# Performance work log

Measured on AMD Instinct MI355X. Metric: run time of the kernel, lower is better.

Reference implementation:

```python
import jax, jax.numpy as jnp
import numpy as np

D_MODEL = 1024
NUM_HEADS = 16
HEAD_DIM = D_MODEL // NUM_HEADS


def setup_inputs() -> dict:
    key = jax.random.key(0)
    ks = jax.random.split(key, 5)
    B, S = 4, 2048
    scale = 0.02
    return {
        "x": jax.random.normal(ks[0], (B, S, D_MODEL), dtype=jnp.float32),
        "q_proj_weight": jax.random.normal(ks[1], (D_MODEL, D_MODEL), dtype=jnp.float32) * scale,
        "k_proj_weight": jax.random.normal(ks[2], (D_MODEL, D_MODEL), dtype=jnp.float32) * scale,
        "v_proj_weight": jax.random.normal(ks[3], (D_MODEL, D_MODEL), dtype=jnp.float32) * scale,
        "o_proj_weight": jax.random.normal(ks[4], (D_MODEL, D_MODEL), dtype=jnp.float32) * scale,
    }


def reference(x, q_proj_weight, k_proj_weight, v_proj_weight, o_proj_weight):
    B, S, _ = x.shape
    H, Dh = NUM_HEADS, HEAD_DIM

    def proj(w):  # [B,S,d_model] x [d_k,d_in] -> [B,H,S,Dh]
        p = jnp.einsum('bsd,kd->bsk', x, w)
        return p.reshape(B, S, H, Dh).transpose(0, 2, 1, 3)

    q = proj(q_proj_weight)
    k = proj(k_proj_weight)
    v = proj(v_proj_weight)

    scores = jnp.einsum('bhqd,bhkd->bhqk', q, k) / jnp.sqrt(jnp.asarray(Dh, dtype=x.dtype))
    causal = jnp.tril(jnp.ones((S, S), dtype=bool))  # [S,S]
    scores = jnp.where(causal, scores, -jnp.inf)
    attn = jax.nn.softmax(scores, axis=-1)
    out = jnp.einsum('bhqk,bhkd->bhqd', attn, v)  # [B,H,S,Dh]
    out = out.transpose(0, 2, 1, 3).reshape(B, S, D_MODEL)
    return jnp.einsum('bsv,mv->bsm', out, o_proj_weight)
```

## Files before the change

kernel.cpp:

```cpp
#include <hip/hip_runtime.h>
#include <cstdint>
#include <cstddef>

#define NH 16
#define DH 64
#define SEQ 2048
#define DM 1024

typedef __attribute__((ext_vector_type(8))) short short8;
typedef __attribute__((ext_vector_type(4))) float f32x4;

__device__ __forceinline__ unsigned short f2bf(float f) {
  unsigned u = __builtin_bit_cast(unsigned, f);
  u += 0x7fffu + ((u >> 16) & 1u);
  return (unsigned short)(u >> 16);
}

__device__ __forceinline__ void gld_lds16(const void* g, void* l) {
  __builtin_amdgcn_global_load_lds((const __attribute__((address_space(1))) void*)g,
                                   (__attribute__((address_space(3))) void*)l,
                                   16, 0, 0);
}

__global__ __launch_bounds__(256) void cast_all_kernel(const float* __restrict__ x,
                                                       const float* __restrict__ wq,
                                                       const float* __restrict__ wk,
                                                       const float* __restrict__ wv,
                                                       const float* __restrict__ wo,
                                                       unsigned short* __restrict__ xb,
                                                       unsigned short* __restrict__ wqkvb,
                                                       unsigned short* __restrict__ wob) {
  const int bid = blockIdx.x;
  const float* in;
  unsigned short* out;
  int i;
  if (bid < 8192) {
    in = x; out = xb; i = bid * 256 + threadIdx.x;
  } else {
    const int w = (bid - 8192) >> 10;
    i = ((bid - 8192) & 1023) * 256 + threadIdx.x;
    in = (w == 0) ? wq : (w == 1) ? wk : (w == 2) ? wv : wo;
    out = (w < 3) ? (wqkvb + (size_t)w * 1048576) : wob;
  }
  const float4 v = ((const float4*)in)[i];
  ushort4 o;
  o.x = f2bf(v.x); o.y = f2bf(v.y); o.z = f2bf(v.z); o.w = f2bf(v.w);
  ((ushort4*)out)[i] = o;
}

__global__ __launch_bounds__(512, 2) void gemm_qkv256(const unsigned short* __restrict__ A,
                                                      const unsigned short* __restrict__ W,
                                                      unsigned short* __restrict__ qb,
                                                      unsigned short* __restrict__ kb,
                                                      unsigned short* __restrict__ vtb) {
  extern __shared__ __align__(16) char sm[];

  const int t = threadIdx.x;
  const int lane = t & 63;
  const int wave = t >> 6;
  const int quad = lane >> 4;
  const int l16 = lane & 15;
  const int wr = wave >> 2;
  const int wc = wave & 3;

  const int bid = blockIdx.x;
  const int xcd = bid & 7;
  const int idx = bid >> 3;
  const int bm = (xcd * 4 + idx / 12) * 256;
  const int bn = (idx % 12) * 256;
  const int sel = bn >> 10;
  const int bnl = bn & 1023;

  f32x4 acc[8][4];
#pragma unroll
  for (int i = 0; i < 8; ++i)
#pragma unroll
    for (int j = 0; j < 4; ++j) acc[i][j] = {0.0f, 0.0f, 0.0f, 0.0f};

  const int r0s = t >> 3;
  const int g0 = (((t & 7) ^ (r0s & 7)) * 8);
  const unsigned short* aS0 = A + (size_t)(bm + r0s) * DM + g0;
  const unsigned short* aS1 = A + (size_t)(bm + 64 + r0s) * DM + g0;
  const unsigned short* bS0 = W + (size_t)(bn + r0s) * DM + g0;
  const unsigned short* bS1 = W + (size_t)(bn + 64 + r0s) * DM + g0;
  const int t16 = t * 16;

  const int aswz = (quad ^ (l16 & 7)) * 16;
  const int aRd0 = (wr * 128 + l16) * 128 + aswz;
  const int aRd1 = aRd0 ^ 64;
  const int bRd0 = 65536 + (wc * 64 + l16) * 128 + aswz;
  const int bRd1 = bRd0 ^ 64;

#define ST_A(U, TK, PAR)                                                                   \
  {                                                                                        \
    gld_lds16(aS0 + (size_t)(U) * 131072 + (TK) * 64, sm + (PAR) * 32768 + (U) * 16384 + t16); \
    gld_lds16(aS1 + (size_t)(U) * 131072 + (TK) * 64,                                      \
              sm + (PAR) * 32768 + (U) * 16384 + 8192 + t16);                              \
  }
#define ST_B(U, TK, PAR)                                                                   \
  {                                                                                        \
    gld_lds16(bS0 + (size_t)(U) * 131072 + (TK) * 64,                                      \
              sm + 65536 + (PAR) * 32768 + (U) * 16384 + t16);                             \
    gld_lds16(bS1 + (size_t)(U) * 131072 + (TK) * 64,                                      \
              sm + 65536 + (PAR) * 32768 + (U) * 16384 + 8192 + t16);                      \
  }

#define MM(AF, BF, IB, JB)                                                                 \
  _Pragma("unroll")                                                                        \
  for (int i = 0; i < 4; ++i)                                                              \
    _Pragma("unroll")                                                                      \
    for (int j = 0; j < 2; ++j) {                                                          \
      acc[(IB) + i][(JB) + j] = __builtin_amdgcn_mfma_f32_16x16x32_bf16(                   \
          AF[i][0], BF[j][0], acc[(IB) + i][(JB) + j], 0, 0, 0);                           \
      acc[(IB) + i][(JB) + j] = __builtin_amdgcn_mfma_f32_16x16x32_bf16(                   \
          AF[i][1], BF[j][1], acc[(IB) + i][(JB) + j], 0, 0, 0);                           \
    }

#define TILE(T, PAR, SB, SA, VM)                                                           \
  {                                                                                        \
    short8 af0[4][2], af1[4][2], bf0[2][2], bf1[2][2];                                     \
                                          \
    _Pragma("unroll")                                                                      \
    for (int i = 0; i < 4; ++i) {                                                          \
      af0[i][0] = *(const short8*)(sm + (PAR) * 32768 + i * 2048 + aRd0);                  \
      af0[i][1] = *(const short8*)(sm + (PAR) * 32768 + i * 2048 + aRd1);                  \
    }                                                                                      \
    _Pragma("unroll")                                                                      \
    for (int j = 0; j < 2; ++j) {                                                          \
      bf0[j][0] = *(const short8*)(sm + (PAR) * 32768 + j * 2048 + bRd0);                  \
      bf0[j][1] = *(const short8*)(sm + (PAR) * 32768 + j * 2048 + bRd1);                  \
    }                                                                                      \
    if (SB) ST_B(0, (T) + 1, (PAR) ^ 1);                                                   \
    asm volatile("" ::: "memory");                                                         \
    __builtin_amdgcn_s_barrier();                                                          \
    asm volatile("s_waitcnt lgkmcnt(0)" ::: "memory");                                     \
    __builtin_amdgcn_s_setprio(1);                                                         \
    MM(af0, bf0, 0, 0);                                                                    \
    __builtin_amdgcn_s_setprio(0);                                                         \
    asm volatile("" ::: "memory");                                                         \
    __builtin_amdgcn_s_barrier();                                                          \
                                                     \
    _Pragma("unroll")                                                                      \
    for (int i = 0; i < 4; ++i) {                                                          \
      af1[i][0] = *(const short8*)(sm + (PAR) * 32768 + 8192 + i * 2048 + aRd0);           \
      af1[i][1] = *(const short8*)(sm + (PAR) * 32768 + 8192 + i * 2048 + aRd1);           \
    }                                                                                      \
    if (SB) ST_B(1, (T) + 1, (PAR) ^ 1);                                                   \
    asm volatile("" ::: "memory");                                                         \
    __builtin_amdgcn_s_barrier();                                                          \
    asm volatile("s_waitcnt lgkmcnt(0)" ::: "memory");                                     \
    __builtin_amdgcn_s_setprio(1);                                                         \
    MM(af1, bf0, 4, 0);                                                                    \
    __builtin_amdgcn_s_setprio(0);                                                         \
    asm volatile("" ::: "memory");                                                         \
    __builtin_amdgcn_s_barrier();                                                          \
                  \
    _Pragma("unroll")                                                                      \
    for (int j = 0; j < 2; ++j) {                                                          \
      bf1[j][0] = *(const short8*)(sm + (PAR) * 32768 + (2 + j) * 2048 + bRd0);            \
      bf1[j][1] = *(const short8*)(sm + (PAR) * 32768 + (2 + j) * 2048 + bRd1);            \
    }                                                                                      \
    if (SA) ST_A(0, (T) + 2, (PAR));                                                       \
    asm volatile("" ::: "memory");                                                         \
    __builtin_amdgcn_s_barrier();                                                          \
    asm volatile("s_waitcnt lgkmcnt(0)" ::: "memory");                                     \
    __builtin_amdgcn_s_setprio(1);                                                         \
    MM(af1, bf1, 4, 2);                                                                    \
    __builtin_amdgcn_s_setprio(0);                                                         \
    asm volatile("" ::: "memory");                                                         \
    __builtin_amdgcn_s_barrier();                                                          \
               \
    if (SA) ST_A(1, (T) + 2, (PAR));                                                       \
    asm volatile("" ::: "memory");                                                         \
    __builtin_amdgcn_s_barrier();                                                          \
    __builtin_amdgcn_s_setprio(1);                                                         \
    MM(af0, bf1, 0, 2);                                                                    \
    __builtin_amdgcn_s_setprio(0);                                                         \
    if ((VM) == 4) asm volatile("s_waitcnt vmcnt(4)" ::: "memory");                        \
    else if ((VM) == 0) asm volatile("s_waitcnt vmcnt(0)" ::: "memory");                   \
    asm volatile("" ::: "memory");                                                         \
    __builtin_amdgcn_s_barrier();                                                          \
  }

  ST_A(0, 0, 0); ST_A(1, 0, 0);
  ST_B(0, 0, 0); ST_B(1, 0, 0);
  ST_A(0, 1, 1); ST_A(1, 1, 1);
  asm volatile("s_waitcnt vmcnt(4)" ::: "memory");
  __builtin_amdgcn_s_barrier();

#pragma unroll 1
  for (int tp = 0; tp < 7; ++tp) {
    const int T0 = tp * 2;
    TILE(T0, 0, 1, 1, 4)
    TILE(T0 + 1, 1, 1, 1, 4)
  }
  TILE(14, 0, 1, 0, 0)
  TILE(15, 1, 0, 0, -1)

#undef TILE
#undef MM
#undef ST_A
#undef ST_B

  if (sel == 2) {
    __syncthreads();
#pragma unroll
    for (int i = 0; i < 8; ++i) {
#pragma unroll
      for (int j = 0; j < 4; ++j) {
        const int n = wc * 64 + j * 16 + l16;
        const int nrow = n * 512;
        const int cswz = (n & 15) << 5;
        const int mb = wr * 128 + i * 16 + quad * 4;
#pragma unroll
        for (int rp = 0; rp < 2; ++rp) {
          const unsigned lo = f2bf(acc[i][j][rp * 2]);
          const unsigned hi = f2bf(acc[i][j][rp * 2 + 1]);
          const int m0 = mb + rp * 2;
          *(unsigned*)(sm + nrow + ((2 * m0) ^ cswz)) = lo | (hi << 16);
        }
      }
    }
    __syncthreads();
    const int mc = t & 31;
    const int nb0 = t >> 5;
    const int bb = bm >> 11;
    const int sbase = (bm & 2047) + mc * 8;
#pragma unroll
    for (int c = 0; c < 16; ++c) {
      const int n = nb0 + c * 16;
      const f32x4 v = *(const f32x4*)(sm + n * 512 + ((mc * 16) ^ ((n & 15) << 5)));
      const int gcol = bnl + n;
      const int h = gcol >> 6, d = gcol & 63;
      *(f32x4*)(vtb + ((size_t)((bb * NH + h) * DH + d)) * SEQ + sbase) = v;
    }
  } else {
#pragma unroll
    for (int i = 0; i < 8; ++i) {
#pragma unroll
      for (int j = 0; j < 4; ++j) {
#pragma unroll
        for (int r = 0; r < 4; ++r) {
          const int m = bm + wr * 128 + i * 16 + quad * 4 + r;
          const int n = bnl + wc * 64 + j * 16 + l16;
          const float v = acc[i][j][r];
          if (sel == 0) {
            qb[(size_t)m * DM + n] = f2bf(v * 0.125f);
          } else {
            kb[(size_t)m * DM + n] = f2bf(v);
          }
        }
      }
    }
  }
}

__global__ __launch_bounds__(256, 4) void gemm_o(const unsigned short* __restrict__ A,
                                                 const unsigned short* __restrict__ B,
                                                 float* __restrict__ C) {
  __shared__ __align__(16) unsigned short As[128 * 32];
  __shared__ __align__(16) unsigned short Bs[128 * 32];
  const int t = threadIdx.x;
  const int lane = t & 63;
  const int wave = t >> 6;
  const int quad = lane >> 4;
  const int l16 = lane & 15;
  const int wm = (wave >> 1) * 64;
  const int wn = (wave & 1) * 64;

  const int lid = blockIdx.x + 8 * blockIdx.y;
  const int xcd = lid & 7;
  const int idx = lid >> 3;
  const int bm = (xcd * 8 + idx / 8) * 128;
  const int bn = (idx % 8) * 128;

  f32x4 acc[4][4];
#pragma unroll
  for (int i = 0; i < 4; ++i)
#pragma unroll
    for (int j = 0; j < 4; ++j) acc[i][j] = {0.0f, 0.0f, 0.0f, 0.0f};

  const int srow = t >> 2;
  const int sc = (t & 3) ^ ((srow >> 1) & 3);
  const unsigned short* Ag1 = A + (size_t)(bm + srow) * DM + sc * 8;
  const unsigned short* Ag2 = A + (size_t)(bm + srow + 64) * DM + sc * 8;
  const unsigned short* Bg1 = B + (size_t)(bn + srow) * DM + sc * 8;
  const unsigned short* Bg2 = B + (size_t)(bn + srow + 64) * DM + sc * 8;
  const int swz = (l16 >> 1) & 3;

  for (int k0 = 0; k0 < DM; k0 += 32) {
    __syncthreads();
    gld_lds16(Ag1 + k0, As + t * 8);
    gld_lds16(Ag2 + k0, As + t * 8 + 2048);
    gld_lds16(Bg1 + k0, Bs + t * 8);
    gld_lds16(Bg2 + k0, Bs + t * 8 + 2048);
    __syncthreads();
    short8 af[4], bfr[4];
#pragma unroll
    for (int i = 0; i < 4; ++i)
      af[i] = *(const short8*)(As + (wm + i * 16 + l16) * 32 + ((quad ^ swz) * 8));
#pragma unroll
    for (int j = 0; j < 4; ++j)
      bfr[j] = *(const short8*)(Bs + (wn + j * 16 + l16) * 32 + ((quad ^ swz) * 8));
#pragma unroll
    for (int i = 0; i < 4; ++i)
#pragma unroll
      for (int j = 0; j < 4; ++j)
        acc[i][j] = __builtin_amdgcn_mfma_f32_16x16x32_bf16(af[i], bfr[j], acc[i][j], 0, 0, 0);
  }

#pragma unroll
  for (int i = 0; i < 4; ++i)
#pragma unroll
    for (int j = 0; j < 4; ++j)
#pragma unroll
      for (int r = 0; r < 4; ++r) {
        const int m = bm + wm + i * 16 + quad * 4 + r;
        const int n = bn + wn + j * 16 + l16;
        C[(size_t)m * DM + n] = acc[i][j][r];
      }
}

__global__ __launch_bounds__(512) void attn_kernel(const unsigned short* __restrict__ Q,
                                                   const unsigned short* __restrict__ K,
                                                   const unsigned short* __restrict__ Vt,
                                                   unsigned short* __restrict__ O) {
  __shared__ __align__(16) unsigned short Ks[128 * 64];
  __shared__ __align__(16) unsigned short Vs[64 * 128];
  __shared__ __align__(16) unsigned short Ps[8][16 * 136];
  const int t = threadIdx.x;
  const int lane = t & 63;
  const int wave = t >> 6;
  const int quad = lane >> 4;
  const int l16 = lane & 15;
  const int h = blockIdx.y;
  const int b = blockIdx.z;

  const int ksr1 = t >> 3;
  const int ksr2 = (t + 512) >> 3;
  const int koff1 = (b * SEQ + ksr1) * DM + h * 64 + (((t & 7) ^ (ksr1 & 7)) * 8);
  const int koff2 = (b * SEQ + ksr2) * DM + h * 64 + (((t & 7) ^ (ksr2 & 7)) * 8);
  const int vsr1 = t >> 4;
  const int vsr2 = (t + 512) >> 4;
  const int voff1 = ((b * NH + h) * DH + vsr1) * SEQ + (((t & 15) ^ (vsr1 & 15)) * 8);
  const int voff2 = ((b * NH + h) * DH + vsr2) * SEQ + (((t & 15) ^ (vsr2 & 15)) * 8);
  unsigned short* Pw = &Ps[wave][0];
  const int swz = l16 & 7;

#pragma unroll 1
  for (int pass = 0; pass < 2; ++pass) {
    const int qt = (pass == 0) ? (int)blockIdx.x : 15 - (int)blockIdx.x;
    const int qtile = qt * 128;
    const int row_lo = qtile + wave * 16;
    const int row_hi = row_lo + 15;

    const unsigned short* Qrow =
        Q + ((size_t)(b * SEQ + row_lo + l16)) * DM + h * 64;
    const short8 qf0 = *(const short8*)(Qrow + quad * 8);
    const short8 qf1 = *(const short8*)(Qrow + 32 + quad * 8);

    f32x4 o_acc[4];
#pragma unroll
    for (int nb = 0; nb < 4; ++nb) o_acc[nb] = {0.0f, 0.0f, 0.0f, 0.0f};
    float l_r[4] = {0.0f, 0.0f, 0.0f, 0.0f};

    const int ktiles = qt + 1;
    for (int kt = 0; kt < ktiles; ++kt) {
      const int kbase = kt * 128;
      __syncthreads();
      gld_lds16(K + koff1 + (size_t)kbase * DM, Ks + t * 8);
      gld_lds16(K + koff2 + (size_t)kbase * DM, Ks + (t + 512) * 8);
      gld_lds16(Vt + voff1 + kbase, Vs + t * 8);
      gld_lds16(Vt + voff2 + kbase, Vs + (t + 512) * 8);
      __syncthreads();

      if (kbase <= row_hi) {
        f32x4 s_acc[8];
#pragma unroll
        for (int nb = 0; nb < 8; ++nb) {
          s_acc[nb] = {0.0f, 0.0f, 0.0f, 0.0f};
          const short8 kf0 = *(const short8*)(Ks + (nb * 16 + l16) * 64 + ((quad ^ swz) * 8));
          const short8 kf1 = *(const short8*)(Ks + (nb * 16 + l16) * 64 + (((4 | quad) ^ swz) * 8));
          s_acc[nb] = __builtin_amdgcn_mfma_f32_16x16x32_bf16(qf0, kf0, s_acc[nb], 0, 0, 0);
          s_acc[nb] = __builtin_amdgcn_mfma_f32_16x16x32_bf16(qf1, kf1, s_acc[nb], 0, 0, 0);
        }

        const bool need_mask = (kbase + 127 > row_lo);
#pragma unroll
        for (int r = 0; r < 4; ++r) {
          const int qr = row_lo + quad * 4 + r;
#pragma unroll
          for (int nb = 0; nb < 8; ++nb) {
            float p = __expf(s_acc[nb][r]);
            if (need_mask) p = ((kbase + nb * 16 + l16) <= qr) ? p : 0.0f;
            l_r[r] += p;
            const unsigned u = __builtin_bit_cast(unsigned, p);
            Pw[(quad * 4 + r) * 136 + nb * 16 + l16] =
                (unsigned short)((u + 0x8000u) >> 16);
          }
        }

#pragma unroll
        for (int kk = 0; kk < 4; ++kk) {
          const short8 pf = *(const short8*)(Pw + l16 * 136 + kk * 32 + quad * 8);
#pragma unroll
          for (int nb = 0; nb < 4; ++nb) {
            const short8 vf = *(const short8*)(Vs + (nb * 16 + l16) * 128 +
                                               (((kk * 4 + quad) ^ l16) * 8));
            o_acc[nb] = __builtin_amdgcn_mfma_f32_16x16x32_bf16(pf, vf, o_acc[nb], 0, 0, 0);
          }
        }
      }
    }

#pragma unroll
    for (int r = 0; r < 4; ++r) {
      float ls = l_r[r];
      ls += __shfl_xor(ls, 1);
      ls += __shfl_xor(ls, 2);
      ls += __shfl_xor(ls, 4);
      ls += __shfl_xor(ls, 8);
      const float inv_l = 1.0f / ls;
      const int qr = row_lo + quad * 4 + r;
#pragma unroll
      for (int nb = 0; nb < 4; ++nb)
        O[((size_t)(b * SEQ + qr)) * DM + h * 64 + nb * 16 + l16] =
            f2bf(o_acc[nb][r] * inv_l);
    }
  }
}

extern "C" void kernel_launch(void* const* d_in, const int* in_sizes, int n_in,
                              void* d_out, int out_size, void* d_ws, size_t ws_size,
                              hipStream_t stream) {
  const float* x  = (const float*)d_in[0];
  const float* wq = (const float*)d_in[1];
  const float* wk = (const float*)d_in[2];
  const float* wv = (const float*)d_in[3];
  const float* wo = (const float*)d_in[4];

  char* ws = (char*)d_ws;
  unsigned short* xb    = (unsigned short*)(ws);
  unsigned short* wqkvb = (unsigned short*)(ws + 16777216);
  unsigned short* wob   = (unsigned short*)(ws + 23068672);
  unsigned short* qb    = (unsigned short*)(ws + 25165824);
  unsigned short* kb    = (unsigned short*)(ws + 41943040);
  unsigned short* vtb   = (unsigned short*)(ws + 58720256);
  unsigned short* aob   = (unsigned short*)(ws + 75497472);

  static bool s_attr_done = false;
  if (!s_attr_done) {
    hipFuncSetAttribute(reinterpret_cast<const void*>(gemm_qkv256),
                        hipFuncAttributeMaxDynamicSharedMemorySize, 131072);
    s_attr_done = true;
  }

  cast_all_kernel<<<12288, 256, 0, stream>>>(x, wq, wk, wv, wo, xb, wqkvb, wob);

  gemm_qkv256<<<dim3(384), dim3(512), 131072, stream>>>(xb, wqkvb, qb, kb, vtb);

  attn_kernel<<<dim3(8, NH, 4), 512, 0, stream>>>(qb, kb, vtb, aob);

  gemm_o<<<dim3(8, 64), 256, 0, stream>>>(aob, wob, (float*)d_out);
}
```

Measured before the change: 244.3 us.

## Double-buffer K/V tiles in attention kernel with async LDS prefetch

```diff
diff --git a/kernel.cpp b/kernel.cpp
--- a/kernel.cpp
+++ b/kernel.cpp
@@ -119,7 +119,6 @@
 #define TILE(T, PAR, SB, SA, VM)                                                           \
   {                                                                                        \
     short8 af0[4][2], af1[4][2], bf0[2][2], bf1[2][2];                                     \
-                                          \
     _Pragma("unroll")                                                                      \
     for (int i = 0; i < 4; ++i) {                                                          \
       af0[i][0] = *(const short8*)(sm + (PAR) * 32768 + i * 2048 + aRd0);                  \
@@ -139,7 +138,6 @@
     __builtin_amdgcn_s_setprio(0);                                                         \
     asm volatile("" ::: "memory");                                                         \
     __builtin_amdgcn_s_barrier();                                                          \
-                                                     \
     _Pragma("unroll")                                                                      \
     for (int i = 0; i < 4; ++i) {                                                          \
       af1[i][0] = *(const short8*)(sm + (PAR) * 32768 + 8192 + i * 2048 + aRd0);           \
@@ -154,7 +152,6 @@
     __builtin_amdgcn_s_setprio(0);                                                         \
     asm volatile("" ::: "memory");                                                         \
     __builtin_amdgcn_s_barrier();                                                          \
-                  \
     _Pragma("unroll")                                                                      \
     for (int j = 0; j < 2; ++j) {                                                          \
       bf1[j][0] = *(const short8*)(sm + (PAR) * 32768 + (2 + j) * 2048 + bRd0);            \
@@ -169,7 +166,6 @@
     __builtin_amdgcn_s_setprio(0);                                                         \
     asm volatile("" ::: "memory");                                                         \
     __builtin_amdgcn_s_barrier();                                                          \
-               \
     if (SA) ST_A(1, (T) + 2, (PAR));                                                       \
     asm volatile("" ::: "memory");                                                         \
     __builtin_amdgcn_s_barrier();                                                          \
@@ -325,9 +321,7 @@
                                                    const unsigned short* __restrict__ K,
                                                    const unsigned short* __restrict__ Vt,
                                                    unsigned short* __restrict__ O) {
-  __shared__ __align__(16) unsigned short Ks[128 * 64];
-  __shared__ __align__(16) unsigned short Vs[64 * 128];
-  __shared__ __align__(16) unsigned short Ps[8][16 * 136];
+  extern __shared__ __align__(16) char asmem[];
   const int t = threadIdx.x;
   const int lane = t & 63;
   const int wave = t >> 6;
@@ -344,15 +338,24 @@
   const int vsr2 = (t + 512) >> 4;
   const int voff1 = ((b * NH + h) * DH + vsr1) * SEQ + (((t & 15) ^ (vsr1 & 15)) * 8);
   const int voff2 = ((b * NH + h) * DH + vsr2) * SEQ + (((t & 15) ^ (vsr2 & 15)) * 8);
-  unsigned short* Pw = &Ps[wave][0];
+  unsigned short* Pw = (unsigned short*)(asmem + 65536) + wave * (16 * 136);
   const int swz = l16 & 7;
+
+#define ATT_STAGE(KB, BUF)                                              \
+  {                                                                     \
+    char* kd = asmem + (BUF) * 16384;                                   \
+    char* vd = asmem + 32768 + (BUF) * 16384;                           \
+    gld_lds16(K + koff1 + (size_t)(KB) * DM, kd + t * 16);              \
+    gld_lds16(K + koff2 + (size_t)(KB) * DM, kd + (t + 512) * 16);      \
+    gld_lds16(Vt + voff1 + (KB), vd + t * 16);                          \
+    gld_lds16(Vt + voff2 + (KB), vd + (t + 512) * 16);                  \
+  }
 
 #pragma unroll 1
   for (int pass = 0; pass < 2; ++pass) {
     const int qt = (pass == 0) ? (int)blockIdx.x : 15 - (int)blockIdx.x;
     const int qtile = qt * 128;
     const int row_lo = qtile + wave * 16;
-    const int row_hi = row_lo + 15;
 
     const unsigned short* Qrow =
         Q + ((size_t)(b * SEQ + row_lo + l16)) * DM + h * 64;
@@ -365,52 +368,59 @@
     float l_r[4] = {0.0f, 0.0f, 0.0f, 0.0f};
 
     const int ktiles = qt + 1;
+    ATT_STAGE(0, 0);
+#pragma unroll 1
     for (int kt = 0; kt < ktiles; ++kt) {
       const int kbase = kt * 128;
-      __syncthreads();
-      gld_lds16(K + koff1 + (size_t)kbase * DM, Ks + t * 8);
-      gld_lds16(K + koff2 + (size_t)kbase * DM, Ks + (t + 512) * 8);
-      gld_lds16(Vt + voff1 + kbase, Vs + t * 8);
-      gld_lds16(Vt + voff2 + kbase, Vs + (t + 512) * 8);
-      __syncthreads();
-
-      if (kbase <= row_hi) {
-        f32x4 s_acc[8];
+      if (kt + 1 < ktiles) {
+        ATT_STAGE((kt + 1) * 128, (kt + 1) & 1);
+        asm volatile("s_waitcnt vmcnt(4)" ::: "memory");
+      } else {
+        asm volatile("s_waitcnt vmcnt(0)" ::: "memory");
+      }
+      __builtin_amdgcn_s_barrier();
+      asm volatile("" ::: "memory");
+      const unsigned short* Ksb = (const unsigned short*)(asmem + (kt & 1) * 16384);
+      const unsigned short* Vsb = (const unsigned short*)(asmem + 32768 + (kt & 1) * 16384);
+
+      f32x4 s_acc[8];
+#pragma unroll
+      for (int nb = 0; nb < 8; ++nb) {
+        s_acc[nb] = {0.0f, 0.0f, 0.0f, 0.0f};
+        const short8 kf0 = *(const short8*)(Ksb + (nb * 16 + l16) * 64 + ((quad ^ swz) * 8));
+        const short8 kf1 = *(const short8*)(Ksb + (nb * 16 + l16) * 64 + (((4 | quad) ^ swz) * 8));
+        s_acc[nb] = __builtin_amdgcn_mfma_f32_16x16x32_bf16(qf0, kf0, s_acc[nb], 0, 0, 0);
+        s_acc[nb] = __builtin_amdgcn_mfma_f32_16x16x32_bf16(qf1, kf1, s_acc[nb], 0, 0, 0);
+      }
+
+      const bool need_mask = (kbase + 127 > row_lo);
+#pragma unroll
+      for (int r = 0; r < 4; ++r) {
+        const int qr = row_lo + quad * 4 + r;
 #pragma unroll
         for (int nb = 0; nb < 8; ++nb) {
-          s_acc[nb] = {0.0f, 0.0f, 0.0f, 0.0f};
-          const short8 kf0 = *(const short8*)(Ks + (nb * 16 + l16) * 64 + ((quad ^ swz) * 8));
-          const short8 kf1 = *(const short8*)(Ks + (nb * 16 + l16) * 64 + (((4 | quad) ^ swz) * 8));
-          s_acc[nb] = __builtin_amdgcn_mfma_f32_16x16x32_bf16(qf0, kf0, s_acc[nb], 0, 0, 0);
-          s_acc[nb] = __builtin_amdgcn_mfma_f32_16x16x32_bf16(qf1, kf1, s_acc[nb], 0, 0, 0);
+          float p = __expf(s_acc[nb][r]);
+          if (need_mask) p = ((kbase + nb * 16 + l16) <= qr) ? p : 0.0f;
+          l_r[r] += p;
+          const unsigned u = __builtin_bit_cast(unsigned, p);
+          Pw[(quad * 4 + r) * 136 + nb * 16 + l16] =
+              (unsigned short)((u + 0x8000u) >> 16);
         }
-
-        const bool need_mask = (kbase + 127 > row_lo);
-#pragma unroll
-        for (int r = 0; r < 4; ++r) {
-          const int qr = row_lo + quad * 4 + r;
-#pragma unroll
-          for (int nb = 0; nb < 8; ++nb) {
-            float p = __expf(s_acc[nb][r]);
-            if (need_mask) p = ((kbase + nb * 16 + l16) <= qr) ? p : 0.0f;
-            l_r[r] += p;
-            const unsigned u = __builtin_bit_cast(unsigned, p);
-            Pw[(quad * 4 + r) * 136 + nb * 16 + l16] =
-                (unsigned short)((u + 0x8000u) >> 16);
-          }
+      }
+
+#pragma unroll
+      for (int kk = 0; kk < 4; ++kk) {
+        const short8 pf = *(const short8*)(Pw + l16 * 136 + kk * 32 + quad * 8);
+#pragma unroll
+        for (int nb = 0; nb < 4; ++nb) {
+          const short8 vf = *(const short8*)(Vsb + (nb * 16 + l16) * 128 +
+                                             (((kk * 4 + quad) ^ l16) * 8));
+          o_acc[nb] = __builtin_amdgcn_mfma_f32_16x16x32_bf16(pf, vf, o_acc[nb], 0, 0, 0);
         }
-
-#pragma unroll
-        for (int kk = 0; kk < 4; ++kk) {
-          const short8 pf = *(const short8*)(Pw + l16 * 136 + kk * 32 + quad * 8);
-#pragma unroll
-          for (int nb = 0; nb < 4; ++nb) {
-            const short8 vf = *(const short8*)(Vs + (nb * 16 + l16) * 128 +
-                                               (((kk * 4 + quad) ^ l16) * 8));
-            o_acc[nb] = __builtin_amdgcn_mfma_f32_16x16x32_bf16(pf, vf, o_acc[nb], 0, 0, 0);
-          }
-        }
-      }
+      }
+
+      asm volatile("" ::: "memory");
+      __builtin_amdgcn_s_barrier();
     }
 
 #pragma unroll
@@ -428,6 +438,7 @@
             f2bf(o_acc[nb][r] * inv_l);
     }
   }
+#undef ATT_STAGE
 }
 
 extern "C" void kernel_launch(void* const* d_in, const int* in_sizes, int n_in,
@@ -452,6 +463,8 @@
   if (!s_attr_done) {
     hipFuncSetAttribute(reinterpret_cast<const void*>(gemm_qkv256),
                         hipFuncAttributeMaxDynamicSharedMemorySize, 131072);
+    hipFuncSetAttribute(reinterpret_cast<const void*>(attn_kernel),
+                        hipFuncAttributeMaxDynamicSharedMemorySize, 100352);
     s_attr_done = true;
   }
 
@@ -459,7 +472,7 @@
 
   gemm_qkv256<<<dim3(384), dim3(512), 131072, stream>>>(xb, wqkvb, qb, kb, vtb);
 
-  attn_kernel<<<dim3(8, NH, 4), 512, 0, stream>>>(qb, kb, vtb, aob);
+  attn_kernel<<<dim3(8, NH, 4), 512, 100352, stream>>>(qb, kb, vtb, aob);
 
   gemm_o<<<dim3(8, 64), 256, 0, stream>>>(aob, wob, (float*)d_out);
 }
```

New measurement: 258.8 us. +5.9%, slower.
